# Kernel tuning notes

Measured on AMD Instinct MI355X. Metric: run time of the kernel, lower is better.

Reference implementation:

```python
import jax, jax.numpy as jnp
import numpy as np

D_MODEL, D_STATE, B, S = 1024, 64, 8, 2048


def setup_inputs() -> dict:
    key = jax.random.key(0)
    ks = jax.random.split(key, 14)
    inp = {"x": jax.random.normal(ks[0], (B, S, D_MODEL), jnp.float32)}
    names = ["cog", "beh", "env", "delta", "Bp", "Cp"]
    for i, n in enumerate(names):
        inp[f"W_{n}"] = jax.random.normal(ks[1 + 2 * i], (D_STATE, D_MODEL), jnp.float32) / np.sqrt(D_MODEL)
        inp[f"b_{n}"] = jnp.zeros((D_STATE,), jnp.float32)
    # torch init is log(|randn|+1e-4); we use strictly-negative A_log so the
    # length-2048 multiplicative recurrence stays finite (A_log is a learned
    # parameter, so its value is free; the math of forward is unchanged).
    inp["A_log"] = -jnp.abs(jax.random.normal(ks[13], (D_STATE, D_STATE), jnp.float32)) - 0.1
    return inp


def reference(x, W_cog, b_cog, W_beh, b_beh, W_env, b_env,
              W_delta, b_delta, W_Bp, b_Bp, W_Cp, b_Cp, A_log):
    # gating terms (computed in the source but never used downstream)
    A_t = (jax.nn.sigmoid(x @ W_cog.T + b_cog)
           * jax.nn.sigmoid(x @ W_beh.T + b_beh)
           * jax.nn.sigmoid(x @ W_env.T + b_env))
    del A_t

    delta = jax.nn.softplus(x @ W_delta.T + b_delta)   # [B,S,N]
    Bt = x @ W_Bp.T + b_Bp                             # [B,S,N]
    Ct = x @ W_Cp.T + b_Cp                             # [B,S,N]
    u = Bt * x[:, :, :D_STATE]                         # [B,S,N]

    # Faithful to torch broadcasting: after step 0 the carried state h is
    # [B,N,N] with h[b,i,j] = exp(A_log[i,j]*delta[b,t,i]) * h_prev[b,i,j] + u[b,t,j]
    def step(h, td):
        d, u_t, c_t = td                               # each [B,N]
        A = jnp.exp(A_log[None, :, :] * d[:, :, None]) # [B,N,N]
        h = A * h + u_t[:, None, :]
        y = jnp.einsum('bj,bij->bi', c_t, h)           # [B,N]
        return h, y

    h0 = jnp.zeros((x.shape[0], D_STATE, D_STATE), x.dtype)
    _, ys = jax.lax.scan(
        step, h0,
        (delta.transpose(1, 0, 2), u.transpose(1, 0, 2), Ct.transpose(1, 0, 2)))
    # torch stacks y_t of shape [B,1,N] along dim=1 -> [B,S,1,N]
    return ys.transpose(1, 0, 2)[:, :, None, :]
```

## Files before the change

### kernel.cpp

```cpp
#include <hip/hip_runtime.h>
#include <math.h>

#define DM   1024
#define DS   64
#define BATCH 8
#define SEQ  2048
#define CL   32
#define NC   64

typedef __bf16 bf16x8 __attribute__((ext_vector_type(8)));
typedef float  f32x4  __attribute__((ext_vector_type(4)));
typedef float  f32x16 __attribute__((ext_vector_type(16)));

#if __has_builtin(__builtin_amdgcn_exp2f)
#define EXP2(v) __builtin_amdgcn_exp2f(v)
#else
#define EXP2(v) __expf(0.69314718056f * (v))
#endif

__global__ __launch_bounds__(256) void wconv_kernel(
    const float* __restrict__ Wd, const float* __restrict__ Wb,
    const float* __restrict__ Wc, __bf16* __restrict__ Wp)
{
    int idx = blockIdx.x * 256 + threadIdx.x;
    int k  = idx & 1023;
    int n  = idx >> 10;
    const float* W = (n < 64) ? Wd : (n < 128 ? Wb : Wc);
    float v = W[(size_t)(n & 63) * DM + k];
    int kt = k >> 5, kk = k & 31;
    Wp[((size_t)kt * 192 + n) * 32 + kk] = (__bf16)v;
}

__global__ __launch_bounds__(256, 1) void proj_mfma(
    const float* __restrict__ x, const __bf16* __restrict__ Wp,
    const float* __restrict__ bd, const float* __restrict__ bb,
    const float* __restrict__ bc,
    float* __restrict__ delta_g, float* __restrict__ u_g,
    float* __restrict__ ct_g)
{
    __shared__ __bf16 sB[2][192 * 72];

    const int tid  = threadIdx.x;
    const int row0 = blockIdx.x * 64;

    const int lane = tid & 63, wv = tid >> 6;
    const int l31  = lane & 31, q = lane >> 5;
    const int mbase = row0 + (wv & 1) * 32;
    const int nhalf = (wv >> 1) * 96;

    const float* xrow = x + (size_t)(mbase + l31) * DM;

    f32x16 acc[3];
    #pragma unroll
    for (int i = 0; i < 3; ++i)
        acc[i] = (f32x16){0,0,0,0,0,0,0,0,0,0,0,0,0,0,0,0};

    float4 aC[8], aN[8];
    uint4  wreg[6];

    #define LOADB(kb) do {                                                    \
        _Pragma("unroll")                                                     \
        for (int it = 0; it < 6; ++it) {                                      \
            int g   = tid + it * 256;                                         \
            int ktl = (it >= 3) ? 1 : 0;                                      \
            int r   = g - ktl * 768;                                          \
            int n   = r >> 2, c4 = r & 3;                                     \
            wreg[it] = *(const uint4*)(                                       \
                Wp + ((size_t)((kb) * 2 + ktl) * 192 + n) * 32 + c4 * 8);     \
        }                                                                     \
    } while (0)
    #define STAGEB(bi) do {                                                   \
        _Pragma("unroll")                                                     \
        for (int it = 0; it < 6; ++it) {                                      \
            int g   = tid + it * 256;                                         \
            int ktl = (it >= 3) ? 1 : 0;                                      \
            int r   = g - ktl * 768;                                          \
            int n   = r >> 2, c4 = r & 3;                                     \
            *(uint4*)&sB[bi][n * 72 + ktl * 32 + c4 * 8] = wreg[it];          \
        }                                                                     \
    } while (0)
    #define LOADA(dst, kb) do {                                               \
        _Pragma("unroll")                                                     \
        for (int s = 0; s < 4; ++s) {                                         \
            dst[2*s]   = *(const float4*)(xrow + (kb)*64 + s*16 + q*8);       \
            dst[2*s+1] = *(const float4*)(xrow + (kb)*64 + s*16 + q*8 + 4);   \
        }                                                                     \
    } while (0)
    #define COMPUTE(bi) do {                                                  \
        _Pragma("unroll")                                                     \
        for (int s = 0; s < 4; ++s) {                                         \
            float4 a0 = aC[2*s], a1 = aC[2*s+1];                              \
            bf16x8 av = {(__bf16)a0.x, (__bf16)a0.y, (__bf16)a0.z,            \
                         (__bf16)a0.w, (__bf16)a1.x, (__bf16)a1.y,            \
                         (__bf16)a1.z, (__bf16)a1.w};                         \
            _Pragma("unroll")                                                 \
            for (int nt = 0; nt < 3; ++nt) {                                  \
                bf16x8 bv = *(const bf16x8*)                                  \
                    &sB[bi][(nhalf + nt*32 + l31) * 72 + s*16 + q*8];         \
                acc[nt] = __builtin_amdgcn_mfma_f32_32x32x16_bf16(            \
                    av, bv, acc[nt], 0, 0, 0);                                \
            }                                                                 \
        }                                                                     \
    } while (0)

    LOADB(0);
    STAGEB(0);
    LOADA(aC, 0);
    __syncthreads();

    int buf = 0;
    for (int kb = 0; kb < 16; ++kb) {
        if (kb < 15) {
            LOADB(kb + 1);
            LOADA(aN, kb + 1);
        }
        COMPUTE(buf);
        if (kb < 15) STAGEB(buf ^ 1);
        __syncthreads();
        if (kb < 15) {
            #pragma unroll
            for (int i = 0; i < 8; ++i) aC[i] = aN[i];
        }
        buf ^= 1;
    }
    #undef LOADB
    #undef STAGEB
    #undef LOADA
    #undef COMPUTE

    #pragma unroll
    for (int nt = 0; nt < 3; ++nt) {
        int gn  = nhalf + nt * 32 + l31;
        int mat = (nhalf + nt * 32) >> 6;
        int col = gn & 63;
        float bias = (mat == 0) ? bd[col] : (mat == 1 ? bb[col] : bc[col]);
        #pragma unroll
        for (int r = 0; r < 16; ++r) {
            int m = mbase + (r & 3) + 8 * (r >> 2) + 4 * q;
            float v = acc[nt][r] + bias;
            if (mat == 0) {
                float sp = (v > 20.f) ? v : __logf(1.f + __expf(v));
                delta_g[(size_t)m * DS + col] = sp;
            } else if (mat == 1) {
                u_g[(size_t)m * DS + col] = v * x[(size_t)m * DM + col];
            } else {
                ct_g[(size_t)m * DS + col] = v;
            }
        }
    }
}

__global__ __launch_bounds__(256) void pass1_kernel(
    const float* __restrict__ delta_g, const float* __restrict__ u_g,
    const float* __restrict__ A_log,
    float* __restrict__ E, float* __restrict__ Dsum)
{
    __shared__ float s_d[CL * 64];
    __shared__ float s_u[CL * 64];
    const int c = blockIdx.x, b = blockIdx.y, tid = threadIdx.x;
    const int t0 = c * CL;

    const float4* dg = (const float4*)(delta_g + ((size_t)b * SEQ + t0) * DS);
    const float4* ug = (const float4*)(u_g     + ((size_t)b * SEQ + t0) * DS);
    #pragma unroll
    for (int it = 0; it < (CL * 64 / 4) / 256; ++it) {
        int f = tid + it * 256;
        ((float4*)s_d)[f] = dg[f];
        ((float4*)s_u)[f] = ug[f];
    }

    const int i  = tid & 63;
    const int jg = tid >> 6;
    float alog[16];
    {
        const float4* ar = (const float4*)(A_log + i * 64 + jg * 16);
        #pragma unroll
        for (int qq = 0; qq < 4; ++qq) {
            float4 v = ar[qq];
            alog[4*qq+0] = v.x * 1.44269504f; alog[4*qq+1] = v.y * 1.44269504f;
            alog[4*qq+2] = v.z * 1.44269504f; alog[4*qq+3] = v.w * 1.44269504f;
        }
    }
    __syncthreads();

    float h[16];
    #pragma unroll
    for (int k = 0; k < 16; ++k) h[k] = 0.f;
    float dsum = 0.f;

    for (int t = 0; t < CL; ++t) {
        float d = s_d[t * 64 + i];
        dsum += d;
        const float* up = s_u + t * 64 + jg * 16;
        #pragma unroll
        for (int k = 0; k < 16; ++k)
            h[k] = EXP2(alog[k] * d) * h[k] + up[k];
    }

    float* eo = E + (((size_t)c * BATCH + b) * 64 + i) * 64 + jg * 16;
    #pragma unroll
    for (int qq = 0; qq < 4; ++qq)
        ((float4*)eo)[qq] = make_float4(h[4*qq], h[4*qq+1], h[4*qq+2], h[4*qq+3]);
    if (jg == 0) Dsum[((size_t)c * BATCH + b) * 64 + i] = dsum;
}

__global__ __launch_bounds__(256) void pass2_kernel(
    const float* __restrict__ A_log, const float* __restrict__ E,
    const float* __restrict__ Dsum, float* __restrict__ Sin)
{
    const int g = blockIdx.x * 256 + threadIdx.x;
    const int b = g >> 12;
    const int e = g & 4095;
    const int i = e >> 6;
    const float al = A_log[e] * 1.44269504f;

    float Eb[8], db[8];
    #pragma unroll
    for (int p = 0; p < 8; ++p) {
        size_t nb = (size_t)p * BATCH + b;
        Eb[p] = E[nb * 4096 + e];
        db[p] = EXP2(al * Dsum[nb * 64 + i]);
    }

    float carry = 0.f;
    #pragma unroll 8
    for (int c = 0; c < NC; ++c) {
        const int s = c & 7;
        float Ec = Eb[s], dc = db[s];
        if (c + 8 < NC) {
            size_t nb = (size_t)(c + 8) * BATCH + b;
            Eb[s] = E[nb * 4096 + e];
            db[s] = EXP2(al * Dsum[nb * 64 + i]);
        }
        Sin[((size_t)c * BATCH + b) * 4096 + e] = carry;
        carry = dc * carry + Ec;
    }
}

__global__ __launch_bounds__(256) void pass3_kernel(
    const float* __restrict__ delta_g, const float* __restrict__ u_g,
    const float* __restrict__ ct_g, const float* __restrict__ A_log,
    const float* __restrict__ Sin, float* __restrict__ out)
{
    __shared__ float s_d[CL * 64];
    __shared__ float s_u[CL * 64];
    __shared__ float s_c[CL * 64];

    const int c = blockIdx.x, b = blockIdx.y, tid = threadIdx.x;
    const int t0 = c * CL;

    const float4* dg = (const float4*)(delta_g + ((size_t)b * SEQ + t0) * DS);
    const float4* ug = (const float4*)(u_g     + ((size_t)b * SEQ + t0) * DS);
    const float4* cg = (const float4*)(ct_g    + ((size_t)b * SEQ + t0) * DS);
    #pragma unroll
    for (int it = 0; it < (CL * 64 / 4) / 256; ++it) {
        int f = tid + it * 256;
        ((float4*)s_d)[f] = dg[f];
        ((float4*)s_u)[f] = ug[f];
        ((float4*)s_c)[f] = cg[f];
    }

    const int i  = tid >> 2;
    const int jg = tid & 3;

    float alog[16];
    {
        const float4* ar = (const float4*)(A_log + i * 64 + jg * 16);
        #pragma unroll
        for (int qq = 0; qq < 4; ++qq) {
            float4 v = ar[qq];
            alog[4*qq+0] = v.x * 1.44269504f; alog[4*qq+1] = v.y * 1.44269504f;
            alog[4*qq+2] = v.z * 1.44269504f; alog[4*qq+3] = v.w * 1.44269504f;
        }
    }

    float h[16];
    {
        const float4* hin = (const float4*)(
            Sin + (((size_t)c * BATCH + b) * 64 + i) * 64 + jg * 16);
        #pragma unroll
        for (int qq = 0; qq < 4; ++qq) {
            float4 v = hin[qq];
            h[4*qq+0] = v.x; h[4*qq+1] = v.y; h[4*qq+2] = v.z; h[4*qq+3] = v.w;
        }
    }
    __syncthreads();

    for (int t = 0; t < CL; ++t) {
        float d = s_d[t * 64 + i];
        const float* up = s_u + t * 64 + jg * 16;
        const float* cp = s_c + t * 64 + jg * 16;
        float part = 0.f;
        #pragma unroll
        for (int k = 0; k < 16; ++k) {
            h[k] = EXP2(alog[k] * d) * h[k] + up[k];
            part += cp[k] * h[k];
        }
        part += __shfl_xor(part, 1);
        part += __shfl_xor(part, 2);
        if (jg == 0)
            out[((size_t)b * SEQ + t0 + t) * DS + i] = part;
    }
}

extern "C" void kernel_launch(void* const* d_in, const int* in_sizes, int n_in,
                              void* d_out, int out_size, void* d_ws, size_t ws_size,
                              hipStream_t stream)
{
    const float* x     = (const float*)d_in[0];
    const float* Wd    = (const float*)d_in[7];
    const float* bd    = (const float*)d_in[8];
    const float* Wb    = (const float*)d_in[9];
    const float* bb    = (const float*)d_in[10];
    const float* Wc    = (const float*)d_in[11];
    const float* bc    = (const float*)d_in[12];
    const float* A_log = (const float*)d_in[13];
    float* out = (float*)d_out;

    float* ws = (float*)d_ws;
    float* delta_g = ws;
    float* u_g     = ws + 1 * 1048576;
    float* ct_g    = ws + 2 * 1048576;
    float* E       = ws + 3 * 1048576;
    float* Sin     = ws + 5 * 1048576;
    float* Dsum    = ws + 7 * 1048576;
    __bf16* Wp     = (__bf16*)E;

    wconv_kernel<<<768, 256, 0, stream>>>(Wd, Wb, Wc, Wp);
    proj_mfma<<<256, 256, 0, stream>>>(
        x, Wp, bd, bb, bc, delta_g, u_g, ct_g);
    pass1_kernel<<<dim3(NC, BATCH), 256, 0, stream>>>(
        delta_g, u_g, A_log, E, Dsum);
    pass2_kernel<<<128, 256, 0, stream>>>(
        A_log, E, Dsum, Sin);
    pass3_kernel<<<dim3(NC, BATCH), 256, 0, stream>>>(
        delta_g, u_g, ct_g, A_log, Sin, out);
}
```

Baseline: 199.5 us.

## Retile projection GEMM to 32-row blocks with 16x16x32 MFMA and LDS-staged A

The projection GEMM block now covers 32 rows instead of 64, doubling the grid to 512 blocks and allowing 2 blocks per CU. Each wave now owns 48 output columns across both 16-row m-tiles using 16x16x32 bf16 MFMAs. The x tile is converted to bf16 once per block and staged in LDS, replacing per-wave fp32 register loads. The goal is better CU occupancy and parallelism on the x read, at the cost of re-reading the weight tile twice as often per row and extra LDS traffic.

```diff
diff --git a/kernel.cpp b/kernel.cpp
--- a/kernel.cpp
+++ b/kernel.cpp
@@ -10,7 +10,6 @@
 
 typedef __bf16 bf16x8 __attribute__((ext_vector_type(8)));
 typedef float  f32x4  __attribute__((ext_vector_type(4)));
-typedef float  f32x16 __attribute__((ext_vector_type(16)));
 
 #if __has_builtin(__builtin_amdgcn_exp2f)
 #define EXP2(v) __builtin_amdgcn_exp2f(v)
@@ -31,120 +30,119 @@
     Wp[((size_t)kt * 192 + n) * 32 + kk] = (__bf16)v;
 }
 
-__global__ __launch_bounds__(256, 1) void proj_mfma(
+__global__ __launch_bounds__(256, 2) void proj_mfma(
     const float* __restrict__ x, const __bf16* __restrict__ Wp,
     const float* __restrict__ bd, const float* __restrict__ bb,
     const float* __restrict__ bc,
     float* __restrict__ delta_g, float* __restrict__ u_g,
     float* __restrict__ ct_g)
 {
-    __shared__ __bf16 sB[2][192 * 72];
+    __shared__ __bf16 sB[2][12288];
+    __shared__ __bf16 sA[2][32 * 72];
 
     const int tid  = threadIdx.x;
-    const int row0 = blockIdx.x * 64;
+    const int row0 = blockIdx.x * 32;
 
     const int lane = tid & 63, wv = tid >> 6;
-    const int l31  = lane & 31, q = lane >> 5;
-    const int mbase = row0 + (wv & 1) * 32;
-    const int nhalf = (wv >> 1) * 96;
-
-    const float* xrow = x + (size_t)(mbase + l31) * DM;
-
-    f32x16 acc[3];
-    #pragma unroll
-    for (int i = 0; i < 3; ++i)
-        acc[i] = (f32x16){0,0,0,0,0,0,0,0,0,0,0,0,0,0,0,0};
-
-    float4 aC[8], aN[8];
+    const int l15  = lane & 15, quad = lane >> 4;
+    const int nbase = wv * 48;
+
+    const int am = tid >> 3;
+    const int ak = tid & 7;
+    const float* xga = x + (size_t)(row0 + am) * DM + ak * 8;
+
+    f32x4 acc[2][3];
+    #pragma unroll
+    for (int mt = 0; mt < 2; ++mt)
+        #pragma unroll
+        for (int nt = 0; nt < 3; ++nt)
+            acc[mt][nt] = (f32x4){0.f, 0.f, 0.f, 0.f};
+
     uint4  wreg[6];
+    float4 areg[2];
 
     #define LOADB(kb) do {                                                    \
         _Pragma("unroll")                                                     \
-        for (int it = 0; it < 6; ++it) {                                      \
-            int g   = tid + it * 256;                                         \
-            int ktl = (it >= 3) ? 1 : 0;                                      \
-            int r   = g - ktl * 768;                                          \
-            int n   = r >> 2, c4 = r & 3;                                     \
+        for (int it = 0; it < 6; ++it)                                        \
             wreg[it] = *(const uint4*)(                                       \
-                Wp + ((size_t)((kb) * 2 + ktl) * 192 + n) * 32 + c4 * 8);     \
-        }                                                                     \
+                Wp + (size_t)(kb) * 12288 + (tid + it * 256) * 8);            \
     } while (0)
-    #define STAGEB(bi) do {                                                   \
+    #define LOADA(kb) do {                                                    \
+        areg[0] = *(const float4*)(xga + (kb) * 64);                          \
+        areg[1] = *(const float4*)(xga + (kb) * 64 + 4);                      \
+    } while (0)
+    #define STAGE(bi) do {                                                    \
         _Pragma("unroll")                                                     \
-        for (int it = 0; it < 6; ++it) {                                      \
-            int g   = tid + it * 256;                                         \
-            int ktl = (it >= 3) ? 1 : 0;                                      \
-            int r   = g - ktl * 768;                                          \
-            int n   = r >> 2, c4 = r & 3;                                     \
-            *(uint4*)&sB[bi][n * 72 + ktl * 32 + c4 * 8] = wreg[it];          \
-        }                                                                     \
-    } while (0)
-    #define LOADA(dst, kb) do {                                               \
-        _Pragma("unroll")                                                     \
-        for (int s = 0; s < 4; ++s) {                                         \
-            dst[2*s]   = *(const float4*)(xrow + (kb)*64 + s*16 + q*8);       \
-            dst[2*s+1] = *(const float4*)(xrow + (kb)*64 + s*16 + q*8 + 4);   \
-        }                                                                     \
+        for (int it = 0; it < 6; ++it)                                        \
+            *(uint4*)&sB[bi][(tid + it * 256) * 8] = wreg[it];                \
+        bf16x8 hv = {(__bf16)areg[0].x, (__bf16)areg[0].y,                    \
+                     (__bf16)areg[0].z, (__bf16)areg[0].w,                    \
+                     (__bf16)areg[1].x, (__bf16)areg[1].y,                    \
+                     (__bf16)areg[1].z, (__bf16)areg[1].w};                   \
+        *(bf16x8*)&sA[bi][am * 72 + ak * 8] = hv;                             \
     } while (0)
     #define COMPUTE(bi) do {                                                  \
         _Pragma("unroll")                                                     \
-        for (int s = 0; s < 4; ++s) {                                         \
-            float4 a0 = aC[2*s], a1 = aC[2*s+1];                              \
-            bf16x8 av = {(__bf16)a0.x, (__bf16)a0.y, (__bf16)a0.z,            \
-                         (__bf16)a0.w, (__bf16)a1.x, (__bf16)a1.y,            \
-                         (__bf16)a1.z, (__bf16)a1.w};                         \
+        for (int s = 0; s < 2; ++s) {                                         \
+            bf16x8 af[2];                                                     \
+            _Pragma("unroll")                                                 \
+            for (int mt = 0; mt < 2; ++mt)                                    \
+                af[mt] = *(const bf16x8*)                                     \
+                    &sA[bi][(mt * 16 + l15) * 72 + s * 32 + quad * 8];        \
             _Pragma("unroll")                                                 \
             for (int nt = 0; nt < 3; ++nt) {                                  \
                 bf16x8 bv = *(const bf16x8*)                                  \
-                    &sB[bi][(nhalf + nt*32 + l31) * 72 + s*16 + q*8];         \
-                acc[nt] = __builtin_amdgcn_mfma_f32_32x32x16_bf16(            \
-                    av, bv, acc[nt], 0, 0, 0);                                \
+                    &sB[bi][s * 6144 + (nbase + nt * 16 + l15) * 32           \
+                            + quad * 8];                                      \
+                _Pragma("unroll")                                             \
+                for (int mt = 0; mt < 2; ++mt)                                \
+                    acc[mt][nt] = __builtin_amdgcn_mfma_f32_16x16x32_bf16(    \
+                        af[mt], bv, acc[mt][nt], 0, 0, 0);                    \
             }                                                                 \
         }                                                                     \
     } while (0)
 
     LOADB(0);
-    STAGEB(0);
-    LOADA(aC, 0);
+    LOADA(0);
+    STAGE(0);
     __syncthreads();
 
     int buf = 0;
     for (int kb = 0; kb < 16; ++kb) {
         if (kb < 15) {
             LOADB(kb + 1);
-            LOADA(aN, kb + 1);
+            LOADA(kb + 1);
         }
         COMPUTE(buf);
-        if (kb < 15) STAGEB(buf ^ 1);
+        if (kb < 15) STAGE(buf ^ 1);
         __syncthreads();
-        if (kb < 15) {
-            #pragma unroll
-            for (int i = 0; i < 8; ++i) aC[i] = aN[i];
-        }
         buf ^= 1;
     }
     #undef LOADB
-    #undef STAGEB
     #undef LOADA
+    #undef STAGE
     #undef COMPUTE
 
     #pragma unroll
     for (int nt = 0; nt < 3; ++nt) {
-        int gn  = nhalf + nt * 32 + l31;
-        int mat = (nhalf + nt * 32) >> 6;
+        int gn  = nbase + nt * 16 + l15;
+        int mat = (nbase + nt * 16) >> 6;
         int col = gn & 63;
         float bias = (mat == 0) ? bd[col] : (mat == 1 ? bb[col] : bc[col]);
         #pragma unroll
-        for (int r = 0; r < 16; ++r) {
-            int m = mbase + (r & 3) + 8 * (r >> 2) + 4 * q;
-            float v = acc[nt][r] + bias;
-            if (mat == 0) {
-                float sp = (v > 20.f) ? v : __logf(1.f + __expf(v));
-                delta_g[(size_t)m * DS + col] = sp;
-            } else if (mat == 1) {
-                u_g[(size_t)m * DS + col] = v * x[(size_t)m * DM + col];
-            } else {
-                ct_g[(size_t)m * DS + col] = v;
+        for (int mt = 0; mt < 2; ++mt) {
+            #pragma unroll
+            for (int r = 0; r < 4; ++r) {
+                int m = row0 + mt * 16 + quad * 4 + r;
+                float v = acc[mt][nt][r] + bias;
+                if (mat == 0) {
+                    float sp = (v > 20.f) ? v : __logf(1.f + __expf(v));
+                    delta_g[(size_t)m * DS + col] = sp;
+                } else if (mat == 1) {
+                    u_g[(size_t)m * DS + col] = v * x[(size_t)m * DM + col];
+                } else {
+                    ct_g[(size_t)m * DS + col] = v;
+                }
             }
         }
     }
@@ -327,7 +325,7 @@
     __bf16* Wp     = (__bf16*)E;
 
     wconv_kernel<<<768, 256, 0, stream>>>(Wd, Wb, Wc, Wp);
-    proj_mfma<<<256, 256, 0, stream>>>(
+    proj_mfma<<<512, 256, 0, stream>>>(
         x, Wp, bd, bb, bc, delta_g, u_g, ct_g);
     pass1_kernel<<<dim3(NC, BATCH), 256, 0, stream>>>(
         delta_g, u_g, A_log, E, Dsum);
```

New measurement: 186.9 us. 6.3% less time.
